# Kernel tuning notes

Hardware: AMD Instinct MI355X
Metric: run time of the kernel (lower is better)

Reference implementation:

```python
import jax, jax.numpy as jnp
import numpy as np

DMODEL = 512
NUM_HEADS = 8
HEAD_DIM = DMODEL // NUM_HEADS
ATTN_LEN = 5
BATCH = 4
SEQ = 4096


def kv_roll(t, layer, shift):
    # t: [B, h_sub, T, 1, hd]; replicates tf.pad + tf.roll + concat + slice
    T = t.shape[2]
    dil = 2 ** layer
    p = dil * (ATTN_LEN // 2)
    tp = jnp.pad(t, ((0, 0), (0, 0), (p, p), (0, 0), (0, 0)))
    # circular rolls, concat along the singleton window axis -> [B,h,T+2p,ATTN_LEN,hd]
    rolled = jnp.concatenate(
        [jnp.roll(tp, -i * dil, axis=2) for i in range(shift, ATTN_LEN + shift)],
        axis=3,
    )
    return rolled[:, :, :T]


def setup_inputs() -> dict:
    key = jax.random.key(0)
    ks = jax.random.split(key, 8)
    inputs = jax.random.normal(ks[0], (BATCH, SEQ, DMODEL), dtype=jnp.float32)
    Wq = jax.random.normal(ks[1], (DMODEL, DMODEL), dtype=jnp.float32) * 0.02
    bq = jnp.zeros((DMODEL,), dtype=jnp.float32)
    Wk = jax.random.normal(ks[2], (DMODEL, DMODEL), dtype=jnp.float32) * 0.02
    bk = jnp.zeros((DMODEL,), dtype=jnp.float32)
    Wv = jax.random.normal(ks[3], (DMODEL, DMODEL), dtype=jnp.float32) * 0.02
    bv = jnp.zeros((DMODEL,), dtype=jnp.float32)
    Er = jax.random.normal(ks[4], (NUM_HEADS, HEAD_DIM, ATTN_LEN), dtype=jnp.float32) * 0.05
    return {"inputs": inputs, "Wq": Wq, "bq": bq, "Wk": Wk, "bk": bk,
            "Wv": Wv, "bv": bv, "Er": Er, "layer": 1}


def reference(inputs, Wq, bq, Wk, bk, Wv, bv, Er, layer):
    B, T, D = inputs.shape
    # projections -> [B, H, T, 1, hd]
    def proj(W, b):
        x = inputs @ W + b
        x = x.reshape(B, T, NUM_HEADS, 1, HEAD_DIM)
        return jnp.transpose(x, (0, 2, 1, 3, 4))
    q = proj(Wq, bq)
    k = proj(Wk, bk)
    v = proj(Wv, bv)

    def build_windows(t):
        # per-head-group shifts: heads 0-3 shift 0, head 4 shift -2, head 5 -1, head 6 +1, head 7 +2
        return jnp.concatenate((
            kv_roll(t[:, 0:4], layer, 0),
            kv_roll(t[:, 4:5], layer, -2),
            kv_roll(t[:, 5:6], layer, -1),
            kv_roll(t[:, 6:7], layer, 1),
            kv_roll(t[:, 7:8], layer, 2),
        ), axis=1)  # [B, H, T, ATTN_LEN, hd]

    kw = build_windows(k)
    vw = build_windows(v)

    # qk: [B, H, T, 1, ATTN_LEN]
    qk = jnp.einsum('bhtqd,bhtwd->bhtqw', q, kw)
    # relative positional bias: q @ Er -> [B, H, T, 1, ATTN_LEN]
    qEr = jnp.einsum('bhtqd,hdw->bhtqw', q, Er)
    scale = jnp.sqrt(jnp.float32(HEAD_DIM)).astype(inputs.dtype)
    logits = (qk + qEr) / scale
    mask = (qk == 0).astype(logits.dtype)
    attn = jax.nn.softmax(logits + mask * -10000.0, axis=-1)
    # out: [B, H, T, 1, hd]
    out = jnp.einsum('bhtqw,bhtwd->bhtqd', attn, vw)
    out = jnp.transpose(out[:, :, :, 0, :], (0, 2, 1, 3)).reshape(B, T, D)
    return out, attn
```

## Files before the change

### kernel.cpp

```cpp
#include <hip/hip_runtime.h>
#include <stdint.h>

#define B_ 4
#define T_ 4096
#define D_ 512
#define H_ 8
#define HD_ 64
#define W_ 5
#define M_ (B_*T_)
#define TILE 128
#define HALO 16
#define TMg 160
#define TN 192
#define LSTR 72

#define AS1_OFF 5120
#define BS0_OFF 10240
#define BS1_OFF 16384
#define SH_ELEMS 32256

typedef __attribute__((ext_vector_type(8))) short short8;
typedef __attribute__((ext_vector_type(4))) float floatx4;

__device__ __forceinline__ unsigned short f2bf(float f) {
    unsigned int u = __builtin_bit_cast(unsigned int, f);
    u += 0x7fffu + ((u >> 16) & 1u);
    return (unsigned short)(u >> 16);
}
__device__ __forceinline__ float bf2f(unsigned short s) {
    unsigned int u = ((unsigned int)s) << 16;
    return __builtin_bit_cast(float, u);
}
__device__ __forceinline__ void load8bf(const unsigned short* p, float* f) {
    uint4 d = *(const uint4*)p;
    f[0] = bf2f((unsigned short)(d.x & 0xffffu));
    f[1] = bf2f((unsigned short)(d.x >> 16));
    f[2] = bf2f((unsigned short)(d.y & 0xffffu));
    f[3] = bf2f((unsigned short)(d.y >> 16));
    f[4] = bf2f((unsigned short)(d.z & 0xffffu));
    f[5] = bf2f((unsigned short)(d.z >> 16));
    f[6] = bf2f((unsigned short)(d.w & 0xffffu));
    f[7] = bf2f((unsigned short)(d.w >> 16));
}

__device__ __forceinline__ void async16(const unsigned short* g, unsigned short* l) {
    __builtin_amdgcn_global_load_lds(
        (const __attribute__((address_space(1))) unsigned int*)g,
        (__attribute__((address_space(3))) unsigned int*)l, 16, 0, 0);
}

__global__ __launch_bounds__(256) void prep(const float* __restrict__ x,
                                            const float* __restrict__ Wq,
                                            const float* __restrict__ Wk,
                                            const float* __restrict__ Wv,
                                            unsigned short* __restrict__ xb,
                                            unsigned short* __restrict__ Wt2) {
    int bx = blockIdx.x;
    if (bx < 4096) {
        int i = bx * 256 + threadIdx.x;
        const float4* x4 = (const float4*)x;
        float4 a = x4[2*i], b = x4[2*i + 1];
        uint4 o;
        o.x = (unsigned)f2bf(a.x) | ((unsigned)f2bf(a.y) << 16);
        o.y = (unsigned)f2bf(a.z) | ((unsigned)f2bf(a.w) << 16);
        o.z = (unsigned)f2bf(b.x) | ((unsigned)f2bf(b.y) << 16);
        o.w = (unsigned)f2bf(b.z) | ((unsigned)f2bf(b.w) << 16);
        ((uint4*)xb)[i] = o;
    } else {
        int tid = (bx - 4096) * 256 + threadIdx.x;
        int np = tid % 1536;
        int kc = tid / 1536;
        int h = np / 192, n192 = np % 192;
        int sel = n192 >> 6, ch = n192 & 63;
        int c = h * 64 + ch;
        const float* Wsrc = (sel == 0) ? Wq : ((sel == 1) ? Wk : Wv);
        unsigned short us[8];
#pragma unroll
        for (int j = 0; j < 8; j++)
            us[j] = f2bf(Wsrc[(size_t)(kc*8 + j) * D_ + c]);
        uint4 o;
        o.x = (unsigned)us[0] | ((unsigned)us[1] << 16);
        o.y = (unsigned)us[2] | ((unsigned)us[3] << 16);
        o.z = (unsigned)us[4] | ((unsigned)us[5] << 16);
        o.w = (unsigned)us[6] | ((unsigned)us[7] << 16);
        *(uint4*)(Wt2 + (size_t)np * D_ + kc*8) = o;
    }
}

__global__ __launch_bounds__(512, 4) void fused_qkv_attn(
    const unsigned short* __restrict__ Xb,
    const unsigned short* __restrict__ Wt2,
    const float* __restrict__ bq, const float* __restrict__ bk2,
    const float* __restrict__ bv, const float* __restrict__ Er,
    const int* __restrict__ layer_p,
    float* __restrict__ out,
    float* __restrict__ attn_out)
{
    __shared__ unsigned short SH[SH_ELEMS];
    __shared__ float sEr[HD_ * W_];
    unsigned short* As0 = SH;
    unsigned short* Bs0 = SH + BS0_OFF;
    unsigned short* Qs = SH;
    unsigned short* Ks = SH + TILE * LSTR;
    unsigned short* Vs = SH + (TILE + TMg) * LSTR;

    const int tid = threadIdx.x;
    const int wave = tid >> 6, lane = tid & 63;
    const int tile = blockIdx.x >> 3, h = blockIdx.x & 7;
    const int b = tile >> 5;
    const int t0 = (tile & 31) * TILE;
    const long m0g = (long)b * T_ + t0;

    for (int i = tid; i < HD_ * W_; i += 512)
        sEr[i] = Er[h * HD_ * W_ + i];

    const unsigned short* gsrc[3];
    unsigned short* ldst[3];
    int halfoff[3];
#pragma unroll
    for (int j = 0; j < 3; j++) {
        int q = wave + j * 8;
        if (q < 22) {
            if (q < 10) {
                long grow = m0g - HALO + q*16 + (lane >> 2);
                grow = grow < 0 ? 0 : (grow >= M_ ? M_ - 1 : grow);
                gsrc[j] = Xb + grow * D_ + (lane & 3) * 8;
                ldst[j] = As0 + q * 512;
                halfoff[j] = AS1_OFF;
            } else {
                int q2 = q - 10;
                gsrc[j] = Wt2 + ((size_t)h*TN + q2*16 + (lane >> 2)) * D_ + (lane & 3) * 8;
                ldst[j] = Bs0 + q2 * 512;
                halfoff[j] = BS1_OFF - BS0_OFF;
            }
        }
    }

    const int wm = (wave >> 2) * 80;
    const int wn = (wave & 3) * 48;
    const int qd = lane >> 4, r16 = lane & 15;
    floatx4 acc[5][3] = {};

    for (int kc = 0; kc < D_; kc += 64) {
#pragma unroll
        for (int j = 0; j < 3; j++)
            if (wave + j * 8 < 22) {
                async16(gsrc[j] + kc,      ldst[j]);
                async16(gsrc[j] + kc + 32, ldst[j] + halfoff[j]);
            }
        __syncthreads();
        short8 af[5][2], bf[3][2];
#pragma unroll
        for (int half = 0; half < 2; half++) {
            const unsigned short* Ab = SH + half * AS1_OFF;
            const unsigned short* Bb = SH + BS0_OFF + half * (BS1_OFF - BS0_OFF);
#pragma unroll
            for (int mi = 0; mi < 5; mi++)
                af[mi][half] = __builtin_bit_cast(short8,
                    *(const uint4*)(Ab + (wm + mi*16 + r16)*32 + qd*8));
#pragma unroll
            for (int ni = 0; ni < 3; ni++)
                bf[ni][half] = __builtin_bit_cast(short8,
                    *(const uint4*)(Bb + (wn + ni*16 + r16)*32 + qd*8));
        }
#pragma unroll
        for (int half = 0; half < 2; half++)
#pragma unroll
            for (int mi = 0; mi < 5; mi++)
#pragma unroll
                for (int ni = 0; ni < 3; ni++)
                    acc[mi][ni] = __builtin_amdgcn_mfma_f32_16x16x32_bf16(
                        af[mi][half], bf[ni][half], acc[mi][ni], 0, 0, 0);
        __syncthreads();
    }

#pragma unroll
    for (int ni = 0; ni < 3; ni++) {
        int n192 = wn + ni * 16 + r16;
        int sel = n192 >> 6;
        int ch = n192 & 63;
        float bias = (sel == 0) ? bq[h*64 + ch]
                   : (sel == 1) ? bk2[h*64 + ch] : bv[h*64 + ch];
#pragma unroll
        for (int mi = 0; mi < 5; mi++)
#pragma unroll
            for (int r = 0; r < 4; r++) {
                int l = wm + mi*16 + qd*4 + r;
                unsigned short vb = f2bf(acc[mi][ni][r] + bias);
                if (sel == 0) {
                    if (l >= HALO && l < HALO + TILE)
                        Qs[(l - HALO) * LSTR + ch] = vb;
                } else if (sel == 1) {
                    Ks[l * LSTR + ch] = vb;
                } else {
                    Vs[l * LSTR + ch] = vb;
                }
            }
    }
    __syncthreads();

    const int dil = 1 << layer_p[0];
    const int sh = (h < 4) ? 0 : (h == 4 ? -2 : (h == 5 ? -1 : (h == 6 ? 1 : 2)));
    const int c8 = tid & 7, g64 = tid >> 3;

#pragma unroll
    for (int p = 0; p < 2; p++) {
        int tl = g64 + p * 64;
        int t = t0 + tl;
        float qf[8]; load8bf(Qs + tl * LSTR + c8 * 8, qf);

        int pos[W_]; bool val[W_]; float s[W_];
#pragma unroll
        for (int w = 0; w < W_; w++) {
            pos[w] = t + (sh + w - 2) * dil;
            val[w] = (pos[w] >= 0) && (pos[w] < T_);
            float a = 0.f;
            if (val[w]) {
                float kf[8]; load8bf(Ks + (pos[w] - t0 + HALO) * LSTR + c8 * 8, kf);
#pragma unroll
                for (int j = 0; j < 8; j++) a = fmaf(qf[j], kf[j], a);
            }
#pragma unroll
            for (int j = 0; j < 8; j++)
                a = fmaf(qf[j], sEr[(c8*8 + j) * W_ + w], a);
            s[w] = a;
        }
#pragma unroll
        for (int off = 4; off > 0; off >>= 1)
#pragma unroll
            for (int w = 0; w < W_; w++)
                s[w] += __shfl_xor(s[w], off, 8);

        float logit[W_], mx = -1e30f;
#pragma unroll
        for (int w = 0; w < W_; w++) {
            logit[w] = val[w] ? s[w] * 0.125f : -1e30f;
            mx = fmaxf(mx, logit[w]);
        }
        float pw[W_], ssum = 0.f;
#pragma unroll
        for (int w = 0; w < W_; w++) {
            pw[w] = val[w] ? __expf(logit[w] - mx) : 0.f;
            ssum += pw[w];
        }
        const float inv = 1.f / ssum;
        float aw[W_];
#pragma unroll
        for (int w = 0; w < W_; w++) aw[w] = pw[w] * inv;

        if (c8 < W_)
            attn_out[((size_t)(b * H_ + h) * T_ + t) * W_ + c8] = aw[c8];

        float of[8] = {0,0,0,0,0,0,0,0};
#pragma unroll
        for (int w = 0; w < W_; w++) {
            if (val[w]) {
                float vf[8]; load8bf(Vs + (pos[w] - t0 + HALO) * LSTR + c8 * 8, vf);
#pragma unroll
                for (int j = 0; j < 8; j++) of[j] = fmaf(aw[w], vf[j], of[j]);
            }
        }
        float* orow = out + ((size_t)b * T_ + t) * D_ + h * HD_ + c8 * 8;
        *(float4*)(orow)     = make_float4(of[0], of[1], of[2], of[3]);
        *(float4*)(orow + 4) = make_float4(of[4], of[5], of[6], of[7]);
    }
}

extern "C" void kernel_launch(void* const* d_in, const int* in_sizes, int n_in,
                              void* d_out, int out_size, void* d_ws, size_t ws_size,
                              hipStream_t stream) {
    const float* x   = (const float*)d_in[0];
    const float* Wq  = (const float*)d_in[1];
    const float* bq  = (const float*)d_in[2];
    const float* Wk  = (const float*)d_in[3];
    const float* bk  = (const float*)d_in[4];
    const float* Wv  = (const float*)d_in[5];
    const float* bv  = (const float*)d_in[6];
    const float* Er  = (const float*)d_in[7];
    const int* layer = (const int*)d_in[8];

    char* ws = (char*)d_ws;
    unsigned short* Xb  = (unsigned short*)ws;
    unsigned short* Wt2 = (unsigned short*)(ws + (size_t)16*1024*1024);

    float* out  = (float*)d_out;
    float* attn = out + (size_t)B_ * T_ * D_;

    prep<<<4096 + 384, 256, 0, stream>>>(x, Wq, Wk, Wv, Xb, Wt2);
    fused_qkv_attn<<<(M_ / TILE) * 8, 512, 0, stream>>>(Xb, Wt2, bq, bk, bv,
                                                        Er, layer, out, attn);
}
```

Before: 151.1 us.

## Double-buffer GEMM K-loop with async prefetch and raise MFMA wave priority

The QKV projection K-loop now runs sixteen 32-wide steps over two ping-pong LDS buffers, issuing the async global-to-LDS copy for the next step before computing the current one. Before, each step loaded a 64-wide chunk and stalled on it. The MFMA block is wrapped in s_setprio to favour math-issuing waves, and the Er load is kept in a register until after the GEMM before it is written to LDS. This removes one barrier-exposed load latency per step, at the cost of more barriers per step and a dependence on the async copies finishing in order.

Result: slower. 155.4 us (+2.8%).

```diff
diff --git a/kernel.cpp b/kernel.cpp
--- a/kernel.cpp
+++ b/kernel.cpp
@@ -14,9 +14,8 @@
 #define TN 192
 #define LSTR 72
 
-#define AS1_OFF 5120
-#define BS0_OFF 10240
-#define BS1_OFF 16384
+#define STEP_ 11264
+#define BOFF_ 5120
 #define SH_ELEMS 32256
 
 typedef __attribute__((ext_vector_type(8))) short short8;
@@ -98,8 +97,6 @@
 {
     __shared__ unsigned short SH[SH_ELEMS];
     __shared__ float sEr[HD_ * W_];
-    unsigned short* As0 = SH;
-    unsigned short* Bs0 = SH + BS0_OFF;
     unsigned short* Qs = SH;
     unsigned short* Ks = SH + TILE * LSTR;
     unsigned short* Vs = SH + (TILE + TMg) * LSTR;
@@ -111,12 +108,11 @@
     const int t0 = (tile & 31) * TILE;
     const long m0g = (long)b * T_ + t0;
 
-    for (int i = tid; i < HD_ * W_; i += 512)
-        sEr[i] = Er[h * HD_ * W_ + i];
-
-    const unsigned short* gsrc[3];
-    unsigned short* ldst[3];
-    int halfoff[3];
+    float erv = 0.f;
+    if (tid < HD_ * W_) erv = Er[h * HD_ * W_ + tid];
+
+    const unsigned short* gsrc[3] = {Xb, Xb, Xb};
+    int ldoff[3] = {0, 0, 0};
 #pragma unroll
     for (int j = 0; j < 3; j++) {
         int q = wave + j * 8;
@@ -125,52 +121,56 @@
                 long grow = m0g - HALO + q*16 + (lane >> 2);
                 grow = grow < 0 ? 0 : (grow >= M_ ? M_ - 1 : grow);
                 gsrc[j] = Xb + grow * D_ + (lane & 3) * 8;
-                ldst[j] = As0 + q * 512;
-                halfoff[j] = AS1_OFF;
+                ldoff[j] = q * 512;
             } else {
                 int q2 = q - 10;
                 gsrc[j] = Wt2 + ((size_t)h*TN + q2*16 + (lane >> 2)) * D_ + (lane & 3) * 8;
-                ldst[j] = Bs0 + q2 * 512;
-                halfoff[j] = BS1_OFF - BS0_OFF;
-            }
-        }
-    }
+                ldoff[j] = BOFF_ + q2 * 512;
+            }
+        }
+    }
+
+    auto issue = [&](int ss) {
+        unsigned short* bb = SH + (ss & 1) * STEP_;
+#pragma unroll
+        for (int j = 0; j < 3; j++)
+            if (wave + j * 8 < 22)
+                async16(gsrc[j] + ss * 32, bb + ldoff[j]);
+    };
 
     const int wm = (wave >> 2) * 80;
     const int wn = (wave & 3) * 48;
     const int qd = lane >> 4, r16 = lane & 15;
     floatx4 acc[5][3] = {};
 
-    for (int kc = 0; kc < D_; kc += 64) {
-#pragma unroll
-        for (int j = 0; j < 3; j++)
-            if (wave + j * 8 < 22) {
-                async16(gsrc[j] + kc,      ldst[j]);
-                async16(gsrc[j] + kc + 32, ldst[j] + halfoff[j]);
-            }
-        __syncthreads();
-        short8 af[5][2], bf[3][2];
-#pragma unroll
-        for (int half = 0; half < 2; half++) {
-            const unsigned short* Ab = SH + half * AS1_OFF;
-            const unsigned short* Bb = SH + BS0_OFF + half * (BS1_OFF - BS0_OFF);
-#pragma unroll
-            for (int mi = 0; mi < 5; mi++)
-                af[mi][half] = __builtin_bit_cast(short8,
-                    *(const uint4*)(Ab + (wm + mi*16 + r16)*32 + qd*8));
+    issue(0);
+    __syncthreads();
+
+    #pragma unroll
+    for (int s = 0; s < 16; s++) {
+        if (s < 15) issue(s + 1);
+
+        const unsigned short* bufA = SH + (s & 1) * STEP_;
+        const unsigned short* bufB = bufA + BOFF_;
+        short8 af[5], bfr[3];
+#pragma unroll
+        for (int mi = 0; mi < 5; mi++)
+            af[mi] = __builtin_bit_cast(short8,
+                *(const uint4*)(bufA + (wm + mi*16 + r16)*32 + qd*8));
+#pragma unroll
+        for (int ni = 0; ni < 3; ni++)
+            bfr[ni] = __builtin_bit_cast(short8,
+                *(const uint4*)(bufB + (wn + ni*16 + r16)*32 + qd*8));
+
+        __builtin_amdgcn_s_setprio(1);
+#pragma unroll
+        for (int mi = 0; mi < 5; mi++)
 #pragma unroll
             for (int ni = 0; ni < 3; ni++)
-                bf[ni][half] = __builtin_bit_cast(short8,
-                    *(const uint4*)(Bb + (wn + ni*16 + r16)*32 + qd*8));
-        }
-#pragma unroll
-        for (int half = 0; half < 2; half++)
-#pragma unroll
-            for (int mi = 0; mi < 5; mi++)
-#pragma unroll
-                for (int ni = 0; ni < 3; ni++)
-                    acc[mi][ni] = __builtin_amdgcn_mfma_f32_16x16x32_bf16(
-                        af[mi][half], bf[ni][half], acc[mi][ni], 0, 0, 0);
+                acc[mi][ni] = __builtin_amdgcn_mfma_f32_16x16x32_bf16(
+                    af[mi], bfr[ni], acc[mi][ni], 0, 0, 0);
+        __builtin_amdgcn_s_setprio(0);
+
         __syncthreads();
     }
 
@@ -197,6 +197,7 @@
                 }
             }
     }
+    if (tid < HD_ * W_) sEr[tid] = erv;
     __syncthreads();
 
     const int dil = 1 << layer_p[0];
```
